# Performance work log

Measured on AMD Instinct MI355X. Metric: run time of the kernel, lower is better.

Reference implementation:

```python
import jax, jax.numpy as jnp
import numpy as np

TOPK = 13
ALPHA = 1.0
BETA = 6.0
NUM_CLASSES = 80
EPS = 1e-9


def _make_boxes(key, shape, max_half):
    # shape = (..., 4): build valid x1y1x2y2 boxes inside a 640x640 image
    kc, ks = jax.random.split(key)
    centers = jax.random.uniform(kc, shape[:-1] + (2,), minval=30.0, maxval=610.0)
    halves = jax.random.uniform(ks, shape[:-1] + (2,), minval=2.0, maxval=max_half)
    return jnp.concatenate([centers - halves, centers + halves], axis=-1)


def setup_inputs() -> dict:
    key = jax.random.key(0)
    k1, k2, k3, k4, k5 = jax.random.split(key, 5)
    B, L, C, n = 16, 8400, NUM_CLASSES, 128
    pred_scores = jax.random.uniform(k1, (B, L, C), dtype=jnp.float32)
    pred_bboxes = _make_boxes(k2, (B, L, 4), 60.0)
    anchor_points = jax.random.uniform(k3, (L, 2), minval=0.0, maxval=640.0)
    gt_labels = jax.random.randint(k4, (B, n), 0, C, dtype=jnp.int32)
    gt_bboxes = _make_boxes(k5, (B, n, 4), 120.0)
    pad_gt_mask = jnp.ones((B, n, 1), dtype=jnp.float32)
    return {"pred_scores": pred_scores, "pred_bboxes": pred_bboxes,
            "anchor_points": anchor_points, "gt_labels": gt_labels,
            "gt_bboxes": gt_bboxes, "pad_gt_mask": pad_gt_mask}


def _batch_iou(box1, box2, eps=1e-9):
    # box1: [B, n, 4], box2: [B, L, 4] -> iou [B, n, L]
    b1 = box1[:, :, None]  # [B,n,1,4]
    b2 = box2[:, None]     # [B,1,L,4]
    x1y1 = jnp.maximum(b1[..., 0:2], b2[..., 0:2])
    x2y2 = jnp.minimum(b1[..., 2:4], b2[..., 2:4])
    overlap = jnp.prod(jnp.clip(x2y2 - x1y1, 0.0), axis=-1)
    area1 = jnp.prod(jnp.clip(b1[..., 2:4] - b1[..., 0:2], 0.0), axis=-1)
    area2 = jnp.prod(jnp.clip(b2[..., 2:4] - b2[..., 0:2], 0.0), axis=-1)
    return overlap / (area1 + area2 - overlap + eps)


def _points_in_bboxes(points, bboxes, eps=EPS):
    # points: [L,2], bboxes: [B,n,4] -> [B,n,L] float
    x = points[None, None, :, 0]
    y = points[None, None, :, 1]
    xmin = bboxes[..., 0:1]; ymin = bboxes[..., 1:2]
    xmax = bboxes[..., 2:3]; ymax = bboxes[..., 3:4]
    l = x - xmin; t = y - ymin; r = xmax - x; b = ymax - y
    d = jnp.minimum(jnp.minimum(l, t), jnp.minimum(r, b))
    return (d > eps).astype(bboxes.dtype)


def _gather_topk(metrics, topk, topk_mask):
    # metrics: [B,n,L] -> one-hot membership of per-gt topk anchors [B,n,L]
    L = metrics.shape[-1]
    _, topk_idxs = jax.lax.top_k(metrics, topk)          # [B,n,topk]
    is_in_topk = jax.nn.one_hot(topk_idxs, L, dtype=metrics.dtype).sum(-2)
    return is_in_topk * topk_mask


def reference(pred_scores, pred_bboxes, anchor_points, gt_labels, gt_bboxes, pad_gt_mask):
    B, n, _ = gt_bboxes.shape
    L = pred_bboxes.shape[1]
    # pairwise IoU between gts and predicted boxes: [B,n,L]
    ious = _batch_iou(gt_bboxes, pred_bboxes)
    # per-gt class scores gathered from pred_scores: [B,n,L]
    scores_cl = jnp.transpose(pred_scores, (0, 2, 1))                 # [B,C,L]
    bbox_cls_scores = jnp.take_along_axis(scores_cl, gt_labels[:, :, None].astype(jnp.int32), axis=1)
    # task-aligned metric
    alignment = (bbox_cls_scores ** ALPHA) * (ious ** BETA)
    is_in_gts = _points_in_bboxes(anchor_points, gt_bboxes)           # [B,n,L]
    is_in_topk = _gather_topk(alignment * is_in_gts, TOPK, pad_gt_mask)
    mask_positive = is_in_topk * is_in_gts * pad_gt_mask              # [B,n,L]
    # resolve anchors assigned to multiple gts: keep max-IoU gt
    mask_pos_sum = mask_positive.sum(-2)                              # [B,L]
    is_max_iou = jnp.transpose(jax.nn.one_hot(jnp.argmax(ious, axis=-2), n, dtype=ious.dtype), (0, 2, 1))
    mask_positive = jnp.where((mask_pos_sum[:, None, :] > 1), is_max_iou, mask_positive)
    mask_pos_sum = mask_positive.sum(-2)
    # assignment
    assigned_gt_index = jnp.argmax(mask_positive, axis=-2)            # [B,L]
    flat_idx = assigned_gt_index + jnp.arange(B, dtype=assigned_gt_index.dtype)[:, None] * n
    assigned_labels = jnp.reshape(gt_labels, (-1,))[flat_idx]
    assigned_labels = jnp.where(mask_pos_sum > 0, assigned_labels, NUM_CLASSES)
    assigned_bboxes = jnp.reshape(gt_bboxes, (-1, 4))[flat_idx]       # [B,L,4]
    assigned_scores = jax.nn.one_hot(assigned_labels, NUM_CLASSES + 1, dtype=pred_scores.dtype)[..., :NUM_CLASSES]
    # rescale scores by normalized alignment metric
    align_m = alignment * mask_positive
    max_metric = align_m.max(-1, keepdims=True)                       # [B,n,1]
    max_iou = (ious * mask_positive).max(-1, keepdims=True)           # [B,n,1]
    align_m = (align_m / (max_metric + EPS)) * max_iou
    assigned_scores = assigned_scores * align_m.max(-2)[..., None]    # [B,L,C]
    return assigned_labels, assigned_bboxes, assigned_scores
```

## Files before the change

### kernel.cpp

```cpp
#include <hip/hip_runtime.h>
#include <stdint.h>

#define BB    16
#define NGT   128
#define LL    8400
#define CC    80
#define KTOP  13
#define FEPS  1e-9f
#define NCELL 10
#define SLOTS 128
#define LCAP  2048

typedef float vfloat4 __attribute__((ext_vector_type(4)));

__device__ __forceinline__ float iou_f(float4 g, float4 p) {
    float ix0 = fmaxf(g.x, p.x);
    float iy0 = fmaxf(g.y, p.y);
    float ix1 = fminf(g.z, p.z);
    float iy1 = fminf(g.w, p.w);
    float ow = fmaxf(ix1 - ix0, 0.0f);
    float oh = fmaxf(iy1 - iy0, 0.0f);
    float ov = ow * oh;
    float a1 = fmaxf(g.z - g.x, 0.0f) * fmaxf(g.w - g.y, 0.0f);
    float a2 = fmaxf(p.z - p.x, 0.0f) * fmaxf(p.w - p.y, 0.0f);
    return ov / (a1 + a2 - ov + FEPS);
}

#define SORT2(a,b) { unsigned long long _t=(a), _u=(b); (a)=(_u>_t)?_u:_t; (b)=(_u>_t)?_t:_u; }
#define INSERT13(key) do { unsigned long long _k=(key); if (_k > k12) { k12=_k; \
    SORT2(k11,k12) SORT2(k10,k11) SORT2(k9,k10) SORT2(k8,k9) SORT2(k7,k8) \
    SORT2(k6,k7)  SORT2(k5,k6)  SORT2(k4,k5) SORT2(k3,k4) SORT2(k2,k3) \
    SORT2(k1,k2)  SORT2(k0,k1) } } while(0)
#define POP13() { k0=k1;k1=k2;k2=k3;k3=k4;k4=k5;k5=k6;k6=k7;k7=k8;k8=k9;k9=k10;k10=k11;k11=k12;k12=0ull; }

__global__ __launch_bounds__(256) void prep_kernel(
    const float2* __restrict__ anchors,
    int*    __restrict__ bin_cnt,
    int*    __restrict__ bins_j,
    float2* __restrict__ bins_xy,
    int* __restrict__ zero_base,
    int  zero_words)
{
    int blk = blockIdx.x;
    int tid = threadIdx.x;
    if (blk < NCELL * NCELL) {
        __shared__ int lcnt;
        __shared__ int lbin[SLOTS];
        if (tid == 0) lcnt = 0;
        __syncthreads();
        int cy = blk / NCELL, cx = blk % NCELL;
        for (int j = tid; j < LL; j += 256) {
            float2 ap = anchors[j];
            int acx = min(max((int)(ap.x * (1.0f / 64.0f)), 0), NCELL - 1);
            int acy = min(max((int)(ap.y * (1.0f / 64.0f)), 0), NCELL - 1);
            if (acx == cx && acy == cy) {
                int s = atomicAdd(&lcnt, 1);
                if (s < SLOTS) lbin[s] = j;
            }
        }
        __syncthreads();
        if (tid == 0) bin_cnt[blk] = lcnt;
        int n = min(lcnt, SLOTS);
        for (int s = tid; s < n; s += 256) {
            int j = lbin[s];
            bins_j[blk * SLOTS + s]  = j;
            bins_xy[blk * SLOTS + s] = anchors[j];
        }
    } else {
        int t = (blk - NCELL * NCELL) * 256 + tid;
        if (t < zero_words) zero_base[t] = 0;
    }
}

__global__ __launch_bounds__(256) void select_kernel(
    const float*  __restrict__ pred_scores,
    const float4* __restrict__ pred_bboxes,
    const float2* __restrict__ anchors,
    const int*    __restrict__ gt_labels,
    const float4* __restrict__ gt_bboxes,
    const int*    __restrict__ bin_cnt,
    const int*    __restrict__ bins_j,
    const float2* __restrict__ bins_xy,
    int* __restrict__ claim_count,
    int* __restrict__ claimant)
{
    int tid  = threadIdx.x;
    int wave = tid >> 6;
    int lane = tid & 63;
    int blk  = blockIdx.x;
    int row  = (blk & 15) * NGT + (blk >> 4);
    int b    = row >> 7;
    int i_gt = row & (NGT - 1);

    float4 g  = gt_bboxes[row];
    int label = gt_labels[row];
    const float*  sc = pred_scores + (size_t)b * LL * CC + label;
    const float4* pb = pred_bboxes + (size_t)b * LL;

    __shared__ unsigned long long s_list[LCAP];
    __shared__ int s_cnt;
    if (tid == 0) s_cnt = 0;
    __syncthreads();

    int cx0 = min(max((int)(g.x * (1.0f / 64.0f)), 0), NCELL - 1);
    int cy0 = min(max((int)(g.y * (1.0f / 64.0f)), 0), NCELL - 1);
    int cx1 = min(max((int)(g.z * (1.0f / 64.0f)), 0), NCELL - 1);
    int cy1 = min(max((int)(g.w * (1.0f / 64.0f)), 0), NCELL - 1);
    int ncx = cx1 - cx0 + 1;
    int ncells = ncx * (cy1 - cy0 + 1);

    bool ovf = false;
    for (int c = 0; c < ncells; ++c) {
        int cell = (cy0 + c / ncx) * NCELL + (cx0 + c % ncx);
        if (bin_cnt[cell] > SLOTS) ovf = true;
    }

    if (!ovf) {
        for (int c = wave; c < ncells; c += 4) {
            int cell = (cy0 + c / ncx) * NCELL + (cx0 + c % ncx);
            int cnt  = bin_cnt[cell];
            const float2* bxy = bins_xy + cell * SLOTS;
            const int*    bj  = bins_j  + cell * SLOTS;
            for (int s = lane; s < cnt; s += 64) {
                float2 ap = bxy[s];
                float d = fminf(fminf(ap.x - g.x, ap.y - g.y),
                                fminf(g.z - ap.x, g.w - ap.y));
                if (d > FEPS) {
                    int j = bj[s];
                    float4 p = pb[j];
                    float io = iou_f(g, p);
                    if (io > 0.0f) {
                        float sv = sc[(size_t)j * CC];
                        float i2 = io * io;
                        float met = sv * (i2 * i2 * i2);
                        if (met > 0.0f) {
                            int slot = atomicAdd(&s_cnt, 1);
                            if (slot < LCAP)
                                s_list[slot] =
                                    ((unsigned long long)__float_as_uint(met) << 32)
                                    | (unsigned)(~(unsigned)j);
                        }
                    }
                }
            }
        }
    }
    __syncthreads();

    if (wave == 0) {
        unsigned long long k0=0,k1=0,k2=0,k3=0,k4=0,k5=0,k6=0,k7=0,k8=0,k9=0,k10=0,k11=0,k12=0;
        int n = s_cnt;
        if (ovf || n > LCAP) {
            for (int j = lane; j < LL; j += 64) {
                float2 ap = anchors[j];
                float d = fminf(fminf(ap.x - g.x, ap.y - g.y),
                                fminf(g.z - ap.x, g.w - ap.y));
                if (d > FEPS) {
                    float4 p = pb[j];
                    float io = iou_f(g, p);
                    if (io > 0.0f) {
                        float s  = sc[(size_t)j * CC];
                        float i2 = io * io;
                        float met = s * (i2 * i2 * i2);
                        if (met > 0.0f)
                            INSERT13(((unsigned long long)__float_as_uint(met) << 32)
                                     | (unsigned)(~(unsigned)j));
                    }
                }
            }
        } else {
            for (int t = lane; t < n; t += 64)
                INSERT13(s_list[t]);
        }

        unsigned long long winner = 0ull;
        for (int r = 0; r < KTOP; ++r) {
            unsigned long long head = k0;
            unsigned long long m = head;
#pragma unroll
            for (int off = 1; off < 64; off <<= 1) {
                unsigned long long o = __shfl_xor(m, off, 64);
                if (o > m) m = o;
            }
            if (head == m && m != 0ull) POP13();
            if (lane == r) winner = m;
        }

        int jwv = -1;
        if (lane < KTOP && winner != 0ull)
            jwv = (int)(~(unsigned)(winner & 0xFFFFFFFFull));

        bool marked = false;
        for (int r = 0; r < KTOP; ++r) {
            int jv = __shfl(jwv, r, 64);
            if (jv == lane) marked = true;
        }
        unsigned long long nonpos = ~__ballot(marked);
        int P = __popcll(__ballot(jwv >= 0));

        int base = b * LL;
        if (jwv >= 0) {
            atomicAdd(claim_count + base + jwv, 1);
            atomicMax(claimant + base + jwv, i_gt);
        }
        if (lane >= P && lane < KTOP) {
            unsigned long long mask = nonpos;
            for (int t = 0; t < lane - P; ++t) mask &= mask - 1ull;
            int jf = __ffsll(mask) - 1;
            float2 ap = anchors[jf];
            float d = fminf(fminf(ap.x - g.x, ap.y - g.y),
                            fminf(g.z - ap.x, g.w - ap.y));
            if (d > FEPS) {
                atomicAdd(claim_count + base + jf, 1);
                atomicMax(claimant + base + jf, i_gt);
            }
        }
    }
}

__global__ __launch_bounds__(256) void resolve_kernel(
    const float*  __restrict__ pred_scores,
    const float4* __restrict__ pred_bboxes,
    const int*    __restrict__ gt_labels,
    const float4* __restrict__ gt_bboxes,
    const int*    __restrict__ claim_count,
    const int*    __restrict__ claimant,
    int*      __restrict__ assigned_gt,
    float*    __restrict__ align_anchor,
    unsigned* __restrict__ max_metric,
    unsigned* __restrict__ max_iou,
    float*    __restrict__ out_labels,
    float4*   __restrict__ out_bboxes)
{
    int b = blockIdx.y;
    int j = blockIdx.x * 256 + threadIdx.x;

    __shared__ float4 gbox[NGT];
    __shared__ int    glab[NGT];
    if (threadIdx.x < NGT) {
        gbox[threadIdx.x] = gt_bboxes[b * NGT + threadIdx.x];
        glab[threadIdx.x] = gt_labels[b * NGT + threadIdx.x];
    }
    __syncthreads();
    if (j >= LL) return;

    int idx = b * LL + j;
    int cnt = claim_count[idx];
    int g = -1;
    float4 p = pred_bboxes[(size_t)b * LL + j];

    if (cnt == 1) {
        g = claimant[idx];
    } else if (cnt > 1) {
        float best = -1.0f;
        int   bi   = 0;
        for (int i = 0; i < NGT; ++i) {
            float iou = iou_f(gbox[i], p);
            if (iou > best) { best = iou; bi = i; }
        }
        g = bi;
    }
    assigned_gt[idx] = g;

    int label; float4 bb;
    if (g >= 0) {
        float iou = iou_f(gbox[g], p);
        float s   = pred_scores[((size_t)b * LL + j) * CC + glab[g]];
        float i2  = iou * iou;
        float al  = s * (i2 * i2 * i2);
        align_anchor[idx] = al;
        atomicMax(max_metric + b * NGT + g, __float_as_uint(al));
        atomicMax(max_iou    + b * NGT + g, __float_as_uint(iou));
        label = glab[g];
        bb    = gbox[g];
    } else {
        label = CC;
        bb    = gbox[0];
    }
    out_labels[idx] = (float)label;
    out_bboxes[idx] = bb;
}

__global__ __launch_bounds__(256) void score_kernel(
    const int*    __restrict__ gt_labels,
    const int*    __restrict__ assigned_gt,
    const float*  __restrict__ align_anchor,
    const unsigned* __restrict__ max_metric,
    const unsigned* __restrict__ max_iou,
    float*  __restrict__ out_scores)
{
    __shared__ int   s_lab[64];
    __shared__ float s_f[64];

    if (threadIdx.x < 64) {
        int t = blockIdx.x * 64 + threadIdx.x;
        int b = t / LL;
        int g = assigned_gt[t];
        int label = CC;
        float f = 0.0f;
        if (g >= 0) {
            label = gt_labels[b * NGT + g];
            float mm = __uint_as_float(max_metric[b * NGT + g]);
            float mi = __uint_as_float(max_iou[b * NGT + g]);
            f = align_anchor[t] / (mm + FEPS) * mi;
        }
        s_lab[threadIdx.x] = label;
        s_f[threadIdx.x]   = f;
    }
    __syncthreads();

    vfloat4* outs = (vfloat4*)(out_scores + (size_t)blockIdx.x * 64 * CC);
#pragma unroll
    for (int k = 0; k < 5; ++k) {
        int i = k * 256 + threadIdx.x;
        int anchor = i / (CC / 4);
        int c4     = i % (CC / 4);
        int lab    = s_lab[anchor];
        vfloat4 v = {0.f, 0.f, 0.f, 0.f};
        int rel = lab - c4 * 4;
        if (rel >= 0 && rel < 4) v[rel] = s_f[anchor];
        outs[i] = v;
    }
}

extern "C" void kernel_launch(void* const* d_in, const int* in_sizes, int n_in,
                              void* d_out, int out_size, void* d_ws, size_t ws_size,
                              hipStream_t stream)
{
    const float*  pred_scores = (const float*)d_in[0];
    const float4* pred_bboxes = (const float4*)d_in[1];
    const float2* anchors     = (const float2*)d_in[2];
    const int*    gt_labels   = (const int*)d_in[3];
    const float4* gt_bboxes   = (const float4*)d_in[4];

    char* w = (char*)d_ws;
    int*      claim_count  = (int*)(w);
    int*      claimant     = (int*)(w + 537600);
    unsigned* max_metric   = (unsigned*)(w + 1075200);
    unsigned* max_iou      = (unsigned*)(w + 1083392);
    int*      assigned_gt  = (int*)(w + 1091584);
    float*    align_anchor = (float*)(w + 1629184);
    int*      bin_cnt      = (int*)(w + 2166784);
    int*      bins_j       = (int*)(w + 2167296);
    float2*   bins_xy      = (float2*)(w + 2218496);

    const int ZERO_WORDS = 1091584 / 4;

    float*  out        = (float*)d_out;
    float*  out_labels = out;
    float4* out_bboxes = (float4*)(out + (size_t)BB * LL);
    float*  out_scores = out + (size_t)BB * LL * 5;

    int zero_blocks = (ZERO_WORDS + 255) / 256;
    prep_kernel<<<NCELL * NCELL + zero_blocks, 256, 0, stream>>>(
        anchors, bin_cnt, bins_j, bins_xy, (int*)w, ZERO_WORDS);

    select_kernel<<<BB * NGT, 256, 0, stream>>>(
        pred_scores, pred_bboxes, anchors, gt_labels, gt_bboxes,
        bin_cnt, bins_j, bins_xy, claim_count, claimant);

    dim3 gridC((LL + 255) / 256, BB);
    resolve_kernel<<<gridC, 256, 0, stream>>>(
        pred_scores, pred_bboxes, gt_labels, gt_bboxes,
        claim_count, claimant, assigned_gt, align_anchor, max_metric, max_iou,
        out_labels, out_bboxes);

    score_kernel<<<(BB * LL) / 64, 256, 0, stream>>>(
        gt_labels, assigned_gt, align_anchor, max_metric, max_iou, out_scores);
}
```

Baseline: 86.02 us.

## Zero score output in prep kernel and scatter only positive scores

The dense score tensor is now zeroed with vectorized stores inside the prep kernel, which already runs before selection, instead of being fully written in the final score kernel. The score kernel shrinks to one thread per anchor that writes a single value when the anchor has an assigned gt. The aim is to move the large output write off the critical tail so it overlaps with the small prep work, and to make the last kernel trivially cheap. The cost is that prep now issues about 43 MB of zero writes, and the final kernel does scattered single-float stores.

```diff
diff --git a/kernel.cpp b/kernel.cpp
--- a/kernel.cpp
+++ b/kernel.cpp
@@ -38,11 +38,14 @@
     int*    __restrict__ bin_cnt,
     int*    __restrict__ bins_j,
     float2* __restrict__ bins_xy,
-    int* __restrict__ zero_base,
-    int  zero_words)
+    vfloat4* __restrict__ zero1,
+    int  z1_vec,
+    vfloat4* __restrict__ zero2,
+    int  z2_vec)
 {
     int blk = blockIdx.x;
     int tid = threadIdx.x;
+    const vfloat4 zv = {0.f, 0.f, 0.f, 0.f};
     if (blk < NCELL * NCELL) {
         __shared__ int lcnt;
         __shared__ int lbin[SLOTS];
@@ -67,8 +70,15 @@
             bins_xy[blk * SLOTS + s] = anchors[j];
         }
     } else {
-        int t = (blk - NCELL * NCELL) * 256 + tid;
-        if (t < zero_words) zero_base[t] = 0;
+        int zblk = blk - NCELL * NCELL;
+        int z1_blocks = (z1_vec + 255) / 256;
+        if (zblk < z1_blocks) {
+            int t = zblk * 256 + tid;
+            if (t < z1_vec) zero1[t] = zv;
+        } else {
+            int t = (zblk - z1_blocks) * 256 + tid;
+            if (t < z2_vec) zero2[t] = zv;
+        }
     }
 }
 
@@ -289,37 +299,16 @@
     const unsigned* __restrict__ max_iou,
     float*  __restrict__ out_scores)
 {
-    __shared__ int   s_lab[64];
-    __shared__ float s_f[64];
-
-    if (threadIdx.x < 64) {
-        int t = blockIdx.x * 64 + threadIdx.x;
-        int b = t / LL;
-        int g = assigned_gt[t];
-        int label = CC;
-        float f = 0.0f;
-        if (g >= 0) {
-            label = gt_labels[b * NGT + g];
-            float mm = __uint_as_float(max_metric[b * NGT + g]);
-            float mi = __uint_as_float(max_iou[b * NGT + g]);
-            f = align_anchor[t] / (mm + FEPS) * mi;
-        }
-        s_lab[threadIdx.x] = label;
-        s_f[threadIdx.x]   = f;
-    }
-    __syncthreads();
-
-    vfloat4* outs = (vfloat4*)(out_scores + (size_t)blockIdx.x * 64 * CC);
-#pragma unroll
-    for (int k = 0; k < 5; ++k) {
-        int i = k * 256 + threadIdx.x;
-        int anchor = i / (CC / 4);
-        int c4     = i % (CC / 4);
-        int lab    = s_lab[anchor];
-        vfloat4 v = {0.f, 0.f, 0.f, 0.f};
-        int rel = lab - c4 * 4;
-        if (rel >= 0 && rel < 4) v[rel] = s_f[anchor];
-        outs[i] = v;
+    int t = blockIdx.x * 256 + threadIdx.x;
+    if (t >= BB * LL) return;
+    int b = t / LL;
+    int g = assigned_gt[t];
+    if (g >= 0) {
+        int label = gt_labels[b * NGT + g];
+        float mm = __uint_as_float(max_metric[b * NGT + g]);
+        float mi = __uint_as_float(max_iou[b * NGT + g]);
+        float f = align_anchor[t] / (mm + FEPS) * mi;
+        out_scores[(size_t)t * CC + label] = f;
     }
 }
 
@@ -344,16 +333,18 @@
     int*      bins_j       = (int*)(w + 2167296);
     float2*   bins_xy      = (float2*)(w + 2218496);
 
-    const int ZERO_WORDS = 1091584 / 4;
-
     float*  out        = (float*)d_out;
     float*  out_labels = out;
     float4* out_bboxes = (float4*)(out + (size_t)BB * LL);
     float*  out_scores = out + (size_t)BB * LL * 5;
 
-    int zero_blocks = (ZERO_WORDS + 255) / 256;
-    prep_kernel<<<NCELL * NCELL + zero_blocks, 256, 0, stream>>>(
-        anchors, bin_cnt, bins_j, bins_xy, (int*)w, ZERO_WORDS);
+    const int Z1_VEC = 1091584 / 16;
+    const int Z2_VEC = (BB * LL * CC * 4) / 16;
+    int z1_blocks = (Z1_VEC + 255) / 256;
+    int z2_blocks = (Z2_VEC + 255) / 256;
+    prep_kernel<<<NCELL * NCELL + z1_blocks + z2_blocks, 256, 0, stream>>>(
+        anchors, bin_cnt, bins_j, bins_xy,
+        (vfloat4*)w, Z1_VEC, (vfloat4*)out_scores, Z2_VEC);
 
     select_kernel<<<BB * NGT, 256, 0, stream>>>(
         pred_scores, pred_bboxes, anchors, gt_labels, gt_bboxes,
@@ -365,6 +356,6 @@
         claim_count, claimant, assigned_gt, align_anchor, max_metric, max_iou,
         out_labels, out_bboxes);
 
-    score_kernel<<<(BB * LL) / 64, 256, 0, stream>>>(
+    score_kernel<<<(BB * LL + 255) / 256, 256, 0, stream>>>(
         gt_labels, assigned_gt, align_anchor, max_metric, max_iou, out_scores);
 }
```

After: 82.97 us. -3.5%, faster.
